# Performance work log

Hardware: AMD Instinct MI355X
Metric: run time of the kernel (lower is better)

## Reference

```python
import jax, jax.numpy as jnp
import numpy as np

E = 16        # n_routed_experts
TOP_K = 2
C = 768       # n_embd
I = 1536      # intermediate_size
B, T = 8, 2048


def setup_inputs() -> dict:
    key = jax.random.key(0)
    ks = jax.random.split(key, 9)
    s = 0.02  # init scale
    return {
        "x": jax.random.normal(ks[0], (B, T, C), jnp.float32),
        "w_gate": jax.random.normal(ks[1], (C, E), jnp.float32) * s,
        "expert_bias": jnp.zeros((E,), jnp.float32),
        "wg": jax.random.normal(ks[2], (E, C, I), jnp.float32) * s,
        "wu": jax.random.normal(ks[3], (E, C, I), jnp.float32) * s,
        "wd": jax.random.normal(ks[4], (E, I, C), jnp.float32) * s,
        "swg": jax.random.normal(ks[5], (C, I), jnp.float32) * s,
        "swu": jax.random.normal(ks[6], (C, I), jnp.float32) * s,
        "swd": jax.random.normal(ks[7], (I, C), jnp.float32) * s,
    }


def _expert(x, wg_e, wu_e, wd_e):
    # SwiGLU FFN: down(silu(gate(x)) * up(x))
    return (jax.nn.silu(x @ wg_e) * (x @ wu_e)) @ wd_e


def reference(x, w_gate, expert_bias, wg, wu, wd, swg, swu, swd):
    Bq, Tq, Cq = x.shape
    xf = x.reshape(-1, Cq)  # (N, C)
    n_tok = xf.shape[0]

    # shared experts (1 expert, divided by count=1)
    shared = _expert(xf, swg, swu, swd)

    # router: softmax over (logits + bias), top-k, renormalize
    logits = xf @ w_gate + expert_bias  # (N, E)
    probs = jax.nn.softmax(logits, axis=-1)
    topk_p, topk_i = jax.lax.top_k(probs, TOP_K)
    topk_p = topk_p / jnp.sum(topk_p, axis=-1, keepdims=True)

    # combine weights per expert: zero where expert not selected
    comb = jnp.zeros((n_tok, E), xf.dtype).at[
        jnp.arange(n_tok)[:, None], topk_i
    ].add(topk_p)  # (N, E)

    routed = jnp.zeros_like(xf)
    for e in range(E):  # fixed small expert count
        routed = routed + comb[:, e:e + 1] * _expert(xf, wg[e], wu[e], wd[e])

    return (shared + routed).reshape(Bq, Tq, Cq)
```

## Files before the change

### kernel.cpp

```cpp
#include <hip/hip_runtime.h>

typedef unsigned short u16;
typedef unsigned int u32;
typedef __attribute__((ext_vector_type(4))) float f32x4;
typedef __attribute__((ext_vector_type(8))) short short8;
typedef __attribute__((ext_vector_type(4))) u16 u16x4;
typedef __attribute__((ext_vector_type(8))) u16 u16x8;

#define N_TOK 16384
#define C_DIM 768
#define I_DIM 1536
#define N_EXP 16
#define TM 256
#define BK 64
#define MAXT 208
#define PASS_T 104

#define CI_COUNTS 0
#define CI_STARTS 32
#define CI_NTILES 64
#define CI_TILE_E 128
#define CI_ESLOT 2048
#define CI_TOKW 36864
#define CI_PERM 102400
#define CI_RW 155648

#define XB_OFF  1048576u
#define WGU_OFF 26214400u
#define WDP_OFF 106430464u
#define ACT_OFF 146538496u

#define BAR() asm volatile("s_barrier" ::: "memory")
#define WAITVM(N) asm volatile("s_waitcnt vmcnt(" #N ")" ::: "memory")

__device__ __forceinline__ u16 f2bf(float f) {
  u32 x = __float_as_uint(f);
  return (u16)((x + 0x7FFFu + ((x >> 16) & 1u)) >> 16);
}
__device__ __forceinline__ float bf2f(u16 h) {
  return __uint_as_float(((u32)h) << 16);
}
__device__ __forceinline__ void dma16(const void* g, void* l) {
  __builtin_amdgcn_global_load_lds(
      (const __attribute__((address_space(1))) unsigned int*)g,
      (__attribute__((address_space(3))) unsigned int*)l, 16, 0, 0);
}

__global__ void convert_kernel(const float* __restrict__ wg, const float* __restrict__ wu,
                               const float* __restrict__ wd, const float* __restrict__ swg,
                               const float* __restrict__ swu, const float* __restrict__ swd,
                               u16* __restrict__ wgu, u16* __restrict__ wdp) {
  int bid = blockIdx.x;
  int tid = threadIdx.x, lane = tid & 63, wv = tid >> 6;
  int lsub = lane >> 3, lchk = lane & 7;
  if (bid < 17 * 96) {
    int e = bid / 96, nb = bid % 96;
    int ng = nb * 32 + wv * 8 + lsub;
    int gu = (ng >> 4) & 1;
    int scol = ((ng >> 5) << 4) | (ng & 15);
    const float* src = (e < N_EXP) ? ((gu ? wu : wg) + (size_t)e * C_DIM * I_DIM)
                                   : (gu ? swu : swg);
    u16* drow = wgu + ((size_t)e * (2 * I_DIM) + ng) * C_DIM;
    int c = lchk ^ (ng & 7);
    const float* s0 = src + scol;
    for (int k0 = 0; k0 < C_DIM; k0 += 64) {
      u16x8 o;
#pragma unroll
      for (int j = 0; j < 8; j++) o[j] = f2bf(s0[(size_t)(k0 + c * 8 + j) * I_DIM]);
      *(u16x8*)&drow[k0 + lchk * 8] = o;
    }
  } else {
    int b2 = bid - 17 * 96;
    int e = b2 / 24, nb = b2 % 24;
    const float* src = (e < N_EXP) ? (wd + (size_t)e * I_DIM * C_DIM) : swd;
    u16* dst = wdp + (size_t)e * (I_DIM * C_DIM);
    int ng = nb * 32 + wv * 8 + lsub;
    int c = lchk ^ (ng & 7);
    const float* s0 = src + ng;
    u16* drow = dst + (size_t)ng * I_DIM;
    for (int k0 = 0; k0 < I_DIM; k0 += 64) {
      u16x8 o;
#pragma unroll
      for (int j = 0; j < 8; j++) o[j] = f2bf(s0[(size_t)(k0 + c * 8 + j) * C_DIM]);
      *(u16x8*)&drow[k0 + lchk * 8] = o;
    }
  }
}

__global__ void router_kernel(const float* __restrict__ x, const float* __restrict__ wgate,
                              const float* __restrict__ ebias, int* __restrict__ ctrl,
                              u16* __restrict__ xb) {
  __shared__ float xs[16 * 772];
  __shared__ float wgsT[16 * 772];
  __shared__ float lg[16 * 16];
  int tid = threadIdx.x;
  int tok0 = blockIdx.x * 16;
  const float4* xsrc = (const float4*)(x + (size_t)tok0 * C_DIM);
  const float4* wsrc = (const float4*)wgate;
#pragma unroll
  for (int j = 0; j < 12; j++) {
    int q = tid + j * 256;
    float4 v = xsrc[q];
    int tk = q / 192;
    int c4 = q - tk * 192;
    *(float4*)&xs[tk * 772 + c4 * 4] = v;
    u16x4 o; o.x = f2bf(v.x); o.y = f2bf(v.y); o.z = f2bf(v.z); o.w = f2bf(v.w);
    *(u16x4*)(xb + (size_t)tok0 * C_DIM + (size_t)q * 4) = o;
    float4 w = wsrc[q];
    int c = q >> 2, e0 = (q & 3) * 4;
    wgsT[(e0 + 0) * 772 + c] = w.x;
    wgsT[(e0 + 1) * 772 + c] = w.y;
    wgsT[(e0 + 2) * 772 + c] = w.z;
    wgsT[(e0 + 3) * 772 + c] = w.w;
  }
  __syncthreads();
  int tk = tid >> 4, e = tid & 15;
  float acc = ebias[e];
  const float4* xr = (const float4*)&xs[tk * 772];
  const float4* wr = (const float4*)&wgsT[e * 772];
#pragma unroll 4
  for (int c4 = 0; c4 < 192; c4++) {
    float4 xv = xr[c4], wv = wr[c4];
    acc = fmaf(xv.x, wv.x, fmaf(xv.y, wv.y, fmaf(xv.z, wv.z, fmaf(xv.w, wv.w, acc))));
  }
  lg[tk * 16 + e] = acc;
  __syncthreads();
  if (tid < 16) {
    int n = tok0 + tid;
    float l0 = -1e30f, l1 = -1e30f; int i0 = 0, i1 = 0;
#pragma unroll
    for (int j = 0; j < 16; j++) {
      float l = lg[tid * 16 + j];
      if (l > l0) { l1 = l0; i1 = i0; l0 = l; i0 = j; }
      else if (l > l1) { l1 = l; i1 = j; }
    }
    float e1 = __expf(l1 - l0);
    float inv = 1.f / (1.f + e1);
    int s0 = atomicAdd(&ctrl[CI_COUNTS + i0], 1);
    int s1 = atomicAdd(&ctrl[CI_COUNTS + i1], 1);
    ctrl[CI_ESLOT + 2 * n]     = (i0 << 24) | s0;
    ctrl[CI_ESLOT + 2 * n + 1] = (i1 << 24) | s1;
    float* tw = (float*)(ctrl + CI_TOKW);
    tw[2 * n] = inv; tw[2 * n + 1] = e1 * inv;
  }
}

__global__ void tiles_kernel(int* __restrict__ ctrl) {
  if (threadIdx.x != 0) return;
  int cnt[17];
#pragma unroll
  for (int e = 0; e < 16; e++) cnt[e] = ctrl[CI_COUNTS + e];
  cnt[16] = N_TOK;
  ctrl[CI_COUNTS + 16] = N_TOK;
  int cur = 0, T = 0;
  for (int e = 0; e <= 16; e++) {
    ctrl[CI_STARTS + e] = cur;
    int nt = (cnt[e] + TM - 1) >> 8;
    for (int i = 0; i < nt; i++) ctrl[CI_TILE_E + T++] = e;
    cur += nt << 8;
  }
  ctrl[CI_NTILES] = T;
}

__global__ void scatter_kernel(int* __restrict__ ctrl) {
  int n = blockIdx.x * 256 + threadIdx.x;
  const float* tw = (const float*)(ctrl + CI_TOKW);
  float* rw = (float*)(ctrl + CI_RW);
#pragma unroll
  for (int k = 0; k < 2; k++) {
    int es = ctrl[CI_ESLOT + 2 * n + k];
    int e = es >> 24;
    int slot = es & 0xFFFFFF;
    int row = ctrl[CI_STARTS + e] + slot;
    ctrl[CI_PERM + row] = n;
    rw[row] = tw[2 * n + k];
  }
  int srow = ctrl[CI_STARTS + 16] + n;
  ctrl[CI_PERM + srow] = n;
  rw[srow] = 1.0f;
}

__global__ __launch_bounds__(512, 2)
void gemm1_kernel(const u16* __restrict__ xb, const u16* __restrict__ wgu,
                  u16* __restrict__ act, const int* __restrict__ ctrl, int tile0) {
  __shared__ u16 As[2][256 * 64];
  __shared__ u16 Bs[2][256 * 64];
  int tt = tile0 + blockIdx.x;
  if (tt >= ctrl[CI_NTILES]) return;
  int e = ctrl[CI_TILE_E + tt];
  int row0 = tt << 8;
  int row0l = blockIdx.x << 8;
  int col0c = blockIdx.y << 8;
  int seg = ctrl[CI_STARTS + e];
  bool sh = (e == N_EXP);
  const u16* W = wgu + (size_t)e * (2 * I_DIM * C_DIM);
  int rlim = sh ? 0x7fffffff : (seg + ctrl[CI_COUNTS + e]);
  const int* perm = ctrl + CI_PERM;
  int tid = threadIdx.x;
  int lane = tid & 63, wv = tid >> 6;
  int lsub = lane >> 3, lchk = lane & 7;
  int co = (lchk ^ lsub) * 8;
  const u16* aptr[4];
#pragma unroll
  for (int j = 0; j < 4; j++) {
    int r = row0 + wv * 32 + j * 8 + lsub;
    int tok = sh ? (r - seg) : ((r < rlim) ? perm[r] : 0);
    aptr[j] = xb + (size_t)tok * C_DIM + co;
  }
  const u16* bptr = W + (size_t)(col0c + wv * 32 + lsub) * C_DIM + lchk * 8;
  int ldst = (wv * 32 + lsub) * 64 + lchk * 8;

  f32x4 acc[8][4];
#pragma unroll
  for (int m = 0; m < 8; m++)
#pragma unroll
    for (int n = 0; n < 4; n++) {
      f32x4 z = {0.f, 0.f, 0.f, 0.f};
      acc[m][n] = z;
    }
  int lr = lane & 15, lq = lane >> 4;
  int wr = wv >> 2, wc = wv & 3;

  auto stage = [&](int kt, int slot) {
    int kk = kt * BK;
#pragma unroll
    for (int j = 0; j < 4; j++) dma16(aptr[j] + kk, &As[slot][ldst + j * 512]);
#pragma unroll
    for (int j = 0; j < 4; j++)
      dma16(bptr + (size_t)j * (8 * C_DIM) + kk, &Bs[slot][ldst + j * 512]);
  };

  stage(0, 0);
  stage(1, 1);
  WAITVM(8);
  BAR();
  for (int kt = 0; kt < C_DIM / BK; ++kt) {
    const u16* Ab = As[kt & 1];
    const u16* Bb = Bs[kt & 1];
    __builtin_amdgcn_s_setprio(1);
#pragma unroll
    for (int s = 0; s < 2; ++s) {
      int csh = ((s * 4 + lq) ^ (lr & 7)) * 8;
      short8 bfr[4];
#pragma unroll
      for (int n = 0; n < 4; n++)
        bfr[n] = *(const short8*)&Bb[(wc * 64 + n * 16 + lr) * 64 + csh];
#pragma unroll
      for (int mh = 0; mh < 2; ++mh) {
        short8 afr[4];
#pragma unroll
        for (int mm = 0; mm < 4; mm++)
          afr[mm] = *(const short8*)&Ab[(wr * 128 + mh * 64 + mm * 16 + lr) * 64 + csh];
#pragma unroll
        for (int mm = 0; mm < 4; mm++)
#pragma unroll
          for (int n = 0; n < 4; n++)
            acc[mh * 4 + mm][n] = __builtin_amdgcn_mfma_f32_16x16x32_bf16(
                afr[mm], bfr[n], acc[mh * 4 + mm][n], 0, 0, 0);
      }
    }
    __builtin_amdgcn_s_setprio(0);
    BAR();
    if (kt + 2 < C_DIM / BK) { stage(kt + 2, kt & 1); WAITVM(8); }
    else { WAITVM(0); }
    BAR();
  }
  int cb = (blockIdx.y << 7) + wc * 32;
#pragma unroll
  for (int m = 0; m < 8; m++)
#pragma unroll
    for (int np = 0; np < 2; np++)
#pragma unroll
      for (int rg = 0; rg < 4; rg++) {
        float g = acc[m][2 * np][rg];
        float h = acc[m][2 * np + 1][rg];
        float a = g * (1.f / (1.f + __expf(-g))) * h;
        int r_loc = wr * 128 + m * 16 + lq * 4 + rg;
        act[(size_t)(row0l + r_loc) * I_DIM + cb + np * 16 + lr] = f2bf(a);
      }
}

__global__ __launch_bounds__(512, 2)
void gemm2_kernel(const u16* __restrict__ act, const u16* __restrict__ wdp,
                  float* __restrict__ out, const int* __restrict__ ctrl, int tile0) {
  __shared__ u16 As[2][256 * 64];
  __shared__ u16 Bs[2][128 * 64];
  int tt = tile0 + blockIdx.x;
  if (tt >= ctrl[CI_NTILES]) return;
  int e = ctrl[CI_TILE_E + tt];
  int row0 = tt << 8;
  int row0l = blockIdx.x << 8;
  int col0 = blockIdx.y << 7;
  const u16* D = wdp + (size_t)e * (I_DIM * C_DIM);
  int tid = threadIdx.x;
  int lane = tid & 63, wv = tid >> 6;
  int lsub = lane >> 3, lchk = lane & 7;
  int co = (lchk ^ lsub) * 8;
  const u16* abase = act + (size_t)(row0l + wv * 32 + lsub) * I_DIM + co;
  const u16* bbase = D + (size_t)(col0 + wv * 16 + lsub) * I_DIM + lchk * 8;
  int ldstA = (wv * 32 + lsub) * 64 + lchk * 8;
  int ldstB = (wv * 16 + lsub) * 64 + lchk * 8;

  f32x4 acc[4][4];
#pragma unroll
  for (int m = 0; m < 4; m++)
#pragma unroll
    for (int n = 0; n < 4; n++) {
      f32x4 z = {0.f, 0.f, 0.f, 0.f};
      acc[m][n] = z;
    }
  int lr = lane & 15, lq = lane >> 4;
  int wr = wv >> 1, wc = wv & 1;

  auto stage = [&](int kt, int slot) {
    int kk = kt * BK;
#pragma unroll
    for (int j = 0; j < 4; j++)
      dma16(abase + (size_t)j * (8 * I_DIM) + kk, &As[slot][ldstA + j * 512]);
#pragma unroll
    for (int j = 0; j < 2; j++)
      dma16(bbase + (size_t)j * (8 * I_DIM) + kk, &Bs[slot][ldstB + j * 512]);
  };

  stage(0, 0);
  stage(1, 1);
  WAITVM(6);
  BAR();
  for (int kt = 0; kt < I_DIM / BK; ++kt) {
    const u16* Ab = As[kt & 1];
    const u16* Bb = Bs[kt & 1];
    __builtin_amdgcn_s_setprio(1);
#pragma unroll
    for (int s = 0; s < 2; ++s) {
      int csh = ((s * 4 + lq) ^ (lr & 7)) * 8;
      short8 bfr[4], afr[4];
#pragma unroll
      for (int n = 0; n < 4; n++)
        bfr[n] = *(const short8*)&Bb[(wc * 64 + n * 16 + lr) * 64 + csh];
#pragma unroll
      for (int m = 0; m < 4; m++)
        afr[m] = *(const short8*)&Ab[(wr * 64 + m * 16 + lr) * 64 + csh];
#pragma unroll
      for (int m = 0; m < 4; m++)
#pragma unroll
        for (int n = 0; n < 4; n++)
          acc[m][n] = __builtin_amdgcn_mfma_f32_16x16x32_bf16(afr[m], bfr[n], acc[m][n], 0, 0, 0);
    }
    __builtin_amdgcn_s_setprio(0);
    BAR();
    if (kt + 2 < I_DIM / BK) { stage(kt + 2, kt & 1); WAITVM(6); }
    else { WAITVM(0); }
    BAR();
  }
  const int* perm = ctrl + CI_PERM;
  const float* rw = (const float*)(ctrl + CI_RW);
#pragma unroll
  for (int m = 0; m < 4; m++)
#pragma unroll
    for (int rg = 0; rg < 4; rg++) {
      int rgrow = row0 + wr * 64 + m * 16 + lq * 4 + rg;
      int tokn = perm[rgrow];
      if (tokn < 0) continue;
      float w = rw[rgrow];
      float* obase = out + (size_t)tokn * C_DIM + col0 + wc * 64 + lr;
#pragma unroll
      for (int n = 0; n < 4; n++)
        atomicAdd(obase + n * 16, acc[m][n][rg] * w);
    }
}

extern "C" void kernel_launch(void* const* d_in, const int* in_sizes, int n_in,
                              void* d_out, int out_size, void* d_ws, size_t ws_size,
                              hipStream_t stream) {
  (void)in_sizes; (void)n_in; (void)out_size; (void)ws_size;
  const float* x     = (const float*)d_in[0];
  const float* wgate = (const float*)d_in[1];
  const float* ebias = (const float*)d_in[2];
  const float* wg    = (const float*)d_in[3];
  const float* wu    = (const float*)d_in[4];
  const float* wd    = (const float*)d_in[5];
  const float* swg   = (const float*)d_in[6];
  const float* swu   = (const float*)d_in[7];
  const float* swd   = (const float*)d_in[8];
  float* out = (float*)d_out;
  char* ws = (char*)d_ws;
  int* ctrl = (int*)ws;
  u16* xb  = (u16*)(ws + XB_OFF);
  u16* wgu = (u16*)(ws + WGU_OFF);
  u16* wdp = (u16*)(ws + WDP_OFF);
  u16* act = (u16*)(ws + ACT_OFF);

  hipMemsetAsync(ws, 0, 256, stream);
  hipMemsetAsync(ws + (size_t)CI_PERM * 4, 0xFF, 53248 * 4, stream);
  hipMemsetAsync(d_out, 0, (size_t)N_TOK * C_DIM * 4, stream);
  router_kernel<<<N_TOK / 16, 256, 0, stream>>>(x, wgate, ebias, ctrl, xb);
  tiles_kernel<<<1, 64, 0, stream>>>(ctrl);
  scatter_kernel<<<N_TOK / 256, 256, 0, stream>>>(ctrl);
  convert_kernel<<<17 * 96 + 17 * 24, 256, 0, stream>>>(wg, wu, wd, swg, swu, swd, wgu, wdp);
  for (int p = 0; p < 2; p++) {
    gemm1_kernel<<<dim3(PASS_T, 2 * I_DIM / 256), 512, 0, stream>>>(xb, wgu, act, ctrl, p * PASS_T);
    gemm2_kernel<<<dim3(PASS_T, C_DIM / 128), 512, 0, stream>>>(act, wdp, out, ctrl, p * PASS_T);
  }
}
```

Before: 1.130 ms.

## Split K-tiles into half-stages with interleaved DMA and MFMA, shrink gemm2 tiles

Both GEMM kernels now split each 64-wide K tile into two 32-wide halves in LDS with a new XOR swizzle. LDS fragment reads, async global-to-LDS loads for upcoming halves and MFMA groups are interleaved with finer barriers, so memory traffic overlaps compute. gemm2 moves to 256-thread blocks covering 128-row subtiles, which doubles its grid. The weight conversion drops its pre-swizzle to match the new layout. The finer schedule adds more barriers and carries a risk of LDS hazards.

```diff
diff --git a/kernel.cpp b/kernel.cpp
--- a/kernel.cpp
+++ b/kernel.cpp
@@ -12,7 +12,8 @@
 #define I_DIM 1536
 #define N_EXP 16
 #define TM 256
-#define BK 64
+#define NT1 12
+#define NT2 24
 #define MAXT 208
 #define PASS_T 104
 
@@ -31,6 +32,7 @@
 #define ACT_OFF 146538496u
 
 #define BAR() asm volatile("s_barrier" ::: "memory")
+#define BAR_LG() asm volatile("s_waitcnt lgkmcnt(0)\n\ts_barrier" ::: "memory")
 #define WAITVM(N) asm volatile("s_waitcnt vmcnt(" #N ")" ::: "memory")
 
 __device__ __forceinline__ u16 f2bf(float f) {
@@ -61,12 +63,11 @@
     const float* src = (e < N_EXP) ? ((gu ? wu : wg) + (size_t)e * C_DIM * I_DIM)
                                    : (gu ? swu : swg);
     u16* drow = wgu + ((size_t)e * (2 * I_DIM) + ng) * C_DIM;
-    int c = lchk ^ (ng & 7);
     const float* s0 = src + scol;
     for (int k0 = 0; k0 < C_DIM; k0 += 64) {
       u16x8 o;
 #pragma unroll
-      for (int j = 0; j < 8; j++) o[j] = f2bf(s0[(size_t)(k0 + c * 8 + j) * I_DIM]);
+      for (int j = 0; j < 8; j++) o[j] = f2bf(s0[(size_t)(k0 + lchk * 8 + j) * I_DIM]);
       *(u16x8*)&drow[k0 + lchk * 8] = o;
     }
   } else {
@@ -75,13 +76,12 @@
     const float* src = (e < N_EXP) ? (wd + (size_t)e * I_DIM * C_DIM) : swd;
     u16* dst = wdp + (size_t)e * (I_DIM * C_DIM);
     int ng = nb * 32 + wv * 8 + lsub;
-    int c = lchk ^ (ng & 7);
     const float* s0 = src + ng;
     u16* drow = dst + (size_t)ng * I_DIM;
     for (int k0 = 0; k0 < I_DIM; k0 += 64) {
       u16x8 o;
 #pragma unroll
-      for (int j = 0; j < 8; j++) o[j] = f2bf(s0[(size_t)(k0 + c * 8 + j) * C_DIM]);
+      for (int j = 0; j < 8; j++) o[j] = f2bf(s0[(size_t)(k0 + lchk * 8 + j) * C_DIM]);
       *(u16x8*)&drow[k0 + lchk * 8] = o;
     }
   }
@@ -183,8 +183,8 @@
 __global__ __launch_bounds__(512, 2)
 void gemm1_kernel(const u16* __restrict__ xb, const u16* __restrict__ wgu,
                   u16* __restrict__ act, const int* __restrict__ ctrl, int tile0) {
-  __shared__ u16 As[2][256 * 64];
-  __shared__ u16 Bs[2][256 * 64];
+  __shared__ u16 As[2][2][8192];
+  __shared__ u16 Bs[2][2][8192];
   int tt = tile0 + blockIdx.x;
   if (tt >= ctrl[CI_NTILES]) return;
   int e = ctrl[CI_TILE_E + tt];
@@ -196,19 +196,35 @@
   const u16* W = wgu + (size_t)e * (2 * I_DIM * C_DIM);
   int rlim = sh ? 0x7fffffff : (seg + ctrl[CI_COUNTS + e]);
   const int* perm = ctrl + CI_PERM;
-  int tid = threadIdx.x;
-  int lane = tid & 63, wv = tid >> 6;
-  int lsub = lane >> 3, lchk = lane & 7;
-  int co = (lchk ^ lsub) * 8;
-  const u16* aptr[4];
-#pragma unroll
-  for (int j = 0; j < 4; j++) {
-    int r = row0 + wv * 32 + j * 8 + lsub;
-    int tok = sh ? (r - seg) : ((r < rlim) ? perm[r] : 0);
-    aptr[j] = xb + (size_t)tok * C_DIM + co;
-  }
-  const u16* bptr = W + (size_t)(col0c + wv * 32 + lsub) * C_DIM + lchk * 8;
-  int ldst = (wv * 32 + lsub) * 64 + lchk * 8;
+  int tid = threadIdx.x, lane = tid & 63, wv = tid >> 6;
+  int lr = lane & 15, lq = lane >> 4;
+  int kcl = (lane & 3) ^ ((lane >> 2) & 3);
+  const u16 *aS0, *aS1, *bS0, *bS1;
+  {
+    int r0 = row0 + wv * 16 + (lane >> 2);
+    int r1 = r0 + 128;
+    int t0 = sh ? (r0 - seg) : ((r0 < rlim) ? perm[r0] : 0);
+    int t1 = sh ? (r1 - seg) : ((r1 < rlim) ? perm[r1] : 0);
+    aS0 = xb + (size_t)t0 * C_DIM + kcl * 8;
+    aS1 = xb + (size_t)t1 * C_DIM + kcl * 8;
+    int cb = col0c + wv * 16 + (lane >> 2);
+    bS0 = W + (size_t)cb * C_DIM + kcl * 8;
+    bS1 = W + (size_t)(cb + 128) * C_DIM + kcl * 8;
+  }
+  int dofs = tid * 8;
+
+  auto stA = [&](int kt, int kh) {
+    u16* d = &As[kt & 1][kh][dofs];
+    int ko = kt * 64 + kh * 32;
+    dma16(aS0 + ko, d);
+    dma16(aS1 + ko, d + 4096);
+  };
+  auto stB = [&](int kt, int kh) {
+    u16* d = &Bs[kt & 1][kh][dofs];
+    int ko = kt * 64 + kh * 32;
+    dma16(bS0 + ko, d);
+    dma16(bS1 + ko, d + 4096);
+  };
 
   f32x4 acc[8][4];
 #pragma unroll
@@ -218,88 +234,108 @@
       f32x4 z = {0.f, 0.f, 0.f, 0.f};
       acc[m][n] = z;
     }
-  int lr = lane & 15, lq = lane >> 4;
   int wr = wv >> 2, wc = wv & 3;
-
-  auto stage = [&](int kt, int slot) {
-    int kk = kt * BK;
-#pragma unroll
-    for (int j = 0; j < 4; j++) dma16(aptr[j] + kk, &As[slot][ldst + j * 512]);
-#pragma unroll
-    for (int j = 0; j < 4; j++)
-      dma16(bptr + (size_t)j * (8 * C_DIM) + kk, &Bs[slot][ldst + j * 512]);
-  };
-
-  stage(0, 0);
-  stage(1, 1);
+  short8 afr[4], bfr[4];
+
+  auto rdB = [&](int s, int kh) {
+#pragma unroll
+    for (int n = 0; n < 4; n++) {
+      int i = wc * 64 + n * 16 + lr;
+      bfr[n] = *(const short8*)&Bs[s][kh][i * 32 + ((lq ^ (i & 3)) * 8)];
+    }
+  };
+  auto rdA = [&](int s, int kh, int g) {
+#pragma unroll
+    for (int m = 0; m < 4; m++) {
+      int r = wr * 128 + g * 64 + m * 16 + lr;
+      afr[m] = *(const short8*)&As[s][kh][r * 32 + ((lq ^ (r & 3)) * 8)];
+    }
+  };
+  auto mm = [&](int g) {
+    __builtin_amdgcn_s_setprio(1);
+#pragma unroll
+    for (int m = 0; m < 4; m++)
+#pragma unroll
+      for (int n = 0; n < 4; n++)
+        acc[g * 4 + m][n] = __builtin_amdgcn_mfma_f32_16x16x32_bf16(
+            afr[m], bfr[n], acc[g * 4 + m][n], 0, 0, 0);
+    __builtin_amdgcn_s_setprio(0);
+  };
+
+  stA(0, 0); stB(0, 0); stA(0, 1); stB(0, 1); stA(1, 0); stB(1, 0);
   WAITVM(8);
   BAR();
-  for (int kt = 0; kt < C_DIM / BK; ++kt) {
-    const u16* Ab = As[kt & 1];
-    const u16* Bb = Bs[kt & 1];
-    __builtin_amdgcn_s_setprio(1);
-#pragma unroll
-    for (int s = 0; s < 2; ++s) {
-      int csh = ((s * 4 + lq) ^ (lr & 7)) * 8;
-      short8 bfr[4];
-#pragma unroll
-      for (int n = 0; n < 4; n++)
-        bfr[n] = *(const short8*)&Bb[(wc * 64 + n * 16 + lr) * 64 + csh];
-#pragma unroll
-      for (int mh = 0; mh < 2; ++mh) {
-        short8 afr[4];
-#pragma unroll
-        for (int mm = 0; mm < 4; mm++)
-          afr[mm] = *(const short8*)&Ab[(wr * 128 + mh * 64 + mm * 16 + lr) * 64 + csh];
-#pragma unroll
-        for (int mm = 0; mm < 4; mm++)
-#pragma unroll
-          for (int n = 0; n < 4; n++)
-            acc[mh * 4 + mm][n] = __builtin_amdgcn_mfma_f32_16x16x32_bf16(
-                afr[mm], bfr[n], acc[mh * 4 + mm][n], 0, 0, 0);
+  for (int kt = 0; kt < NT1; ++kt) {
+    int s = kt & 1;
+    rdB(s, 0); rdA(s, 0, 0);
+    if (kt + 1 < NT1) stA(kt + 1, 1);
+    BAR(); mm(0); BAR_LG();
+    rdA(s, 0, 1);
+    if (kt + 1 < NT1) stB(kt + 1, 1);
+    if (kt == NT1 - 1) { WAITVM(0); } else { WAITVM(8); }
+    BAR(); mm(1); BAR_LG();
+    rdB(s, 1); rdA(s, 1, 0);
+    if (kt + 2 < NT1) stA(kt + 2, 0);
+    BAR(); mm(0); BAR_LG();
+    rdA(s, 1, 1);
+    if (kt + 2 < NT1) stB(kt + 2, 0);
+    if (kt < NT1 - 2) { WAITVM(8); } else if (kt == NT1 - 2) { WAITVM(4); }
+    BAR(); mm(1); BAR_LG();
+  }
+  int cbase = (blockIdx.y << 7) + wc * 32;
+#pragma unroll
+  for (int mi = 0; mi < 8; mi++)
+#pragma unroll
+    for (int np = 0; np < 2; np++)
+#pragma unroll
+      for (int rg = 0; rg < 4; rg++) {
+        float g = acc[mi][2 * np][rg];
+        float h = acc[mi][2 * np + 1][rg];
+        float a = g * (1.f / (1.f + __expf(-g))) * h;
+        int r_loc = wr * 128 + mi * 16 + lq * 4 + rg;
+        act[(size_t)(row0l + r_loc) * I_DIM + cbase + np * 16 + lr] = f2bf(a);
       }
-    }
-    __builtin_amdgcn_s_setprio(0);
-    BAR();
-    if (kt + 2 < C_DIM / BK) { stage(kt + 2, kt & 1); WAITVM(8); }
-    else { WAITVM(0); }
-    BAR();
-  }
-  int cb = (blockIdx.y << 7) + wc * 32;
-#pragma unroll
-  for (int m = 0; m < 8; m++)
-#pragma unroll
-    for (int np = 0; np < 2; np++)
-#pragma unroll
-      for (int rg = 0; rg < 4; rg++) {
-        float g = acc[m][2 * np][rg];
-        float h = acc[m][2 * np + 1][rg];
-        float a = g * (1.f / (1.f + __expf(-g))) * h;
-        int r_loc = wr * 128 + m * 16 + lq * 4 + rg;
-        act[(size_t)(row0l + r_loc) * I_DIM + cb + np * 16 + lr] = f2bf(a);
-      }
-}
-
-__global__ __launch_bounds__(512, 2)
+}
+
+__global__ __launch_bounds__(256, 2)
 void gemm2_kernel(const u16* __restrict__ act, const u16* __restrict__ wdp,
                   float* __restrict__ out, const int* __restrict__ ctrl, int tile0) {
-  __shared__ u16 As[2][256 * 64];
-  __shared__ u16 Bs[2][128 * 64];
-  int tt = tile0 + blockIdx.x;
+  __shared__ u16 As[2][2][4096];
+  __shared__ u16 Bs[2][2][4096];
+  int bx = blockIdx.x;
+  int tt = tile0 + (bx >> 1);
   if (tt >= ctrl[CI_NTILES]) return;
   int e = ctrl[CI_TILE_E + tt];
-  int row0 = tt << 8;
-  int row0l = blockIdx.x << 8;
+  int sub = bx & 1;
+  int row0g = (tt << 8) + (sub << 7);
+  int row0l = bx << 7;
   int col0 = blockIdx.y << 7;
   const u16* D = wdp + (size_t)e * (I_DIM * C_DIM);
-  int tid = threadIdx.x;
-  int lane = tid & 63, wv = tid >> 6;
-  int lsub = lane >> 3, lchk = lane & 7;
-  int co = (lchk ^ lsub) * 8;
-  const u16* abase = act + (size_t)(row0l + wv * 32 + lsub) * I_DIM + co;
-  const u16* bbase = D + (size_t)(col0 + wv * 16 + lsub) * I_DIM + lchk * 8;
-  int ldstA = (wv * 32 + lsub) * 64 + lchk * 8;
-  int ldstB = (wv * 16 + lsub) * 64 + lchk * 8;
+  int tid = threadIdx.x, lane = tid & 63, wv = tid >> 6;
+  int lr = lane & 15, lq = lane >> 4;
+  int kcl = (tid & 3) ^ ((tid >> 2) & 3);
+  const u16 *aS0, *aS1, *bS0, *bS1;
+  {
+    int r0 = tid >> 2;
+    aS0 = act + (size_t)(row0l + r0) * I_DIM + kcl * 8;
+    aS1 = act + (size_t)(row0l + r0 + 64) * I_DIM + kcl * 8;
+    bS0 = D + (size_t)(col0 + r0) * I_DIM + kcl * 8;
+    bS1 = D + (size_t)(col0 + r0 + 64) * I_DIM + kcl * 8;
+  }
+  int dofs = tid * 8;
+
+  auto stA = [&](int kt, int kh) {
+    u16* d = &As[kt & 1][kh][dofs];
+    int ko = kt * 64 + kh * 32;
+    dma16(aS0 + ko, d);
+    dma16(aS1 + ko, d + 2048);
+  };
+  auto stB = [&](int kt, int kh) {
+    u16* d = &Bs[kt & 1][kh][dofs];
+    int ko = kt * 64 + kh * 32;
+    dma16(bS0 + ko, d);
+    dma16(bS1 + ko, d + 2048);
+  };
 
   f32x4 acc[4][4];
 #pragma unroll
@@ -309,48 +345,46 @@
       f32x4 z = {0.f, 0.f, 0.f, 0.f};
       acc[m][n] = z;
     }
-  int lr = lane & 15, lq = lane >> 4;
   int wr = wv >> 1, wc = wv & 1;
-
-  auto stage = [&](int kt, int slot) {
-    int kk = kt * BK;
-#pragma unroll
-    for (int j = 0; j < 4; j++)
-      dma16(abase + (size_t)j * (8 * I_DIM) + kk, &As[slot][ldstA + j * 512]);
-#pragma unroll
-    for (int j = 0; j < 2; j++)
-      dma16(bbase + (size_t)j * (8 * I_DIM) + kk, &Bs[slot][ldstB + j * 512]);
-  };
-
-  stage(0, 0);
-  stage(1, 1);
-  WAITVM(6);
+  short8 afr[4], bfr[4];
+
+  auto rdB = [&](int s, int kh) {
+#pragma unroll
+    for (int n = 0; n < 4; n++) {
+      int i = wc * 64 + n * 16 + lr;
+      bfr[n] = *(const short8*)&Bs[s][kh][i * 32 + ((lq ^ (i & 3)) * 8)];
+    }
+  };
+  auto rdA = [&](int s, int kh) {
+#pragma unroll
+    for (int m = 0; m < 4; m++) {
+      int r = wr * 64 + m * 16 + lr;
+      afr[m] = *(const short8*)&As[s][kh][r * 32 + ((lq ^ (r & 3)) * 8)];
+    }
+  };
+  auto mm = [&]() {
+    __builtin_amdgcn_s_setprio(1);
+#pragma unroll
+    for (int m = 0; m < 4; m++)
+#pragma unroll
+      for (int n = 0; n < 4; n++)
+        acc[m][n] = __builtin_amdgcn_mfma_f32_16x16x32_bf16(afr[m], bfr[n], acc[m][n], 0, 0, 0);
+    __builtin_amdgcn_s_setprio(0);
+  };
+
+  stA(0, 0); stB(0, 0); stA(0, 1); stB(0, 1); stA(1, 0); stB(1, 0);
+  WAITVM(8);
   BAR();
-  for (int kt = 0; kt < I_DIM / BK; ++kt) {
-    const u16* Ab = As[kt & 1];
-    const u16* Bb = Bs[kt & 1];
-    __builtin_amdgcn_s_setprio(1);
-#pragma unroll
-    for (int s = 0; s < 2; ++s) {
-      int csh = ((s * 4 + lq) ^ (lr & 7)) * 8;
-      short8 bfr[4], afr[4];
-#pragma unroll
-      for (int n = 0; n < 4; n++)
-        bfr[n] = *(const short8*)&Bb[(wc * 64 + n * 16 + lr) * 64 + csh];
-#pragma unroll
-      for (int m = 0; m < 4; m++)
-        afr[m] = *(const short8*)&Ab[(wr * 64 + m * 16 + lr) * 64 + csh];
-#pragma unroll
-      for (int m = 0; m < 4; m++)
-#pragma unroll
-        for (int n = 0; n < 4; n++)
-          acc[m][n] = __builtin_amdgcn_mfma_f32_16x16x32_bf16(afr[m], bfr[n], acc[m][n], 0, 0, 0);
-    }
-    __builtin_amdgcn_s_setprio(0);
-    BAR();
-    if (kt + 2 < I_DIM / BK) { stage(kt + 2, kt & 1); WAITVM(6); }
-    else { WAITVM(0); }
-    BAR();
+  for (int kt = 0; kt < NT2; ++kt) {
+    int s = kt & 1;
+    rdB(s, 0); rdA(s, 0);
+    if (kt + 1 < NT2) { stA(kt + 1, 1); stB(kt + 1, 1); }
+    if (kt == NT2 - 1) { WAITVM(0); } else { WAITVM(8); }
+    BAR(); mm(); BAR_LG();
+    rdB(s, 1); rdA(s, 1);
+    if (kt + 2 < NT2) { stA(kt + 2, 0); stB(kt + 2, 0); }
+    if (kt < NT2 - 2) { WAITVM(8); } else if (kt == NT2 - 2) { WAITVM(4); }
+    BAR(); mm(); BAR_LG();
   }
   const int* perm = ctrl + CI_PERM;
   const float* rw = (const float*)(ctrl + CI_RW);
@@ -358,7 +392,7 @@
   for (int m = 0; m < 4; m++)
 #pragma unroll
     for (int rg = 0; rg < 4; rg++) {
-      int rgrow = row0 + wr * 64 + m * 16 + lq * 4 + rg;
+      int rgrow = row0g + wr * 64 + m * 16 + lq * 4 + rg;
       int tokn = perm[rgrow];
       if (tokn < 0) continue;
       float w = rw[rgrow];
@@ -399,6 +433,6 @@
   convert_kernel<<<17 * 96 + 17 * 24, 256, 0, stream>>>(wg, wu, wd, swg, swu, swd, wgu, wdp);
   for (int p = 0; p < 2; p++) {
     gemm1_kernel<<<dim3(PASS_T, 2 * I_DIM / 256), 512, 0, stream>>>(xb, wgu, act, ctrl, p * PASS_T);
-    gemm2_kernel<<<dim3(PASS_T, C_DIM / 128), 512, 0, stream>>>(act, wdp, out, ctrl, p * PASS_T);
-  }
-}
+    gemm2_kernel<<<dim3(2 * PASS_T, C_DIM / 128), 256, 0, stream>>>(act, wdp, out, ctrl, p * PASS_T);
+  }
+}
```

Result: faster. 1.078 ms (-4.6%).
